# Kernel tuning notes

Hardware: AMD Instinct MI355X
Metric: run time of the kernel (lower is better)

Reference implementation:

```python
import jax, jax.numpy as jnp
import numpy as np

B, S, D = 1, 2048, 4096
H = 32
Q_RANK, KV_RANK = 1536, 512
NOPE, ROPE, VD = 128, 64, 128
QD = NOPE + ROPE  # 192
EPS = 1e-6
THETA = 10000.0


def setup_inputs() -> dict:
    key = jax.random.key(0)
    ks = jax.random.split(key, 8)
    std = 0.02
    return {
        'hidden_states': jax.random.normal(ks[0], (B, S, D), jnp.float32),
        'Wq_a': jax.random.normal(ks[1], (D, Q_RANK), jnp.float32) * std,
        'q_a_ln_w': jnp.ones((Q_RANK,), jnp.float32),
        'Wq_b': jax.random.normal(ks[2], (Q_RANK, H * QD), jnp.float32) * std,
        'Wkv_a': jax.random.normal(ks[3], (D, KV_RANK + ROPE), jnp.float32) * std,
        'kv_a_ln_w': jnp.ones((KV_RANK,), jnp.float32),
        'Wkv_b': jax.random.normal(ks[4], (KV_RANK, H * (NOPE + VD)), jnp.float32) * std,
        'Wo': jax.random.normal(ks[5], (H * VD, D), jnp.float32) * std,
    }


def _rmsnorm(x, w):
    return x * jax.lax.rsqrt(jnp.mean(x * x, axis=-1, keepdims=True) + EPS) * w


def _rotate_half(x):
    h = x.shape[-1] // 2
    return jnp.concatenate([-x[..., h:], x[..., :h]], axis=-1)


def _apply_rope(x, cos, sin):
    # DeepSeek interleave permutation: view(..., d//2, 2).transpose -> [evens | odds]
    xp = jnp.concatenate([x[..., 0::2], x[..., 1::2]], axis=-1)
    return xp * cos + _rotate_half(xp) * sin


def _mla_forward(hidden_states, Wq_a, q_a_ln_w, Wq_b, Wkv_a, kv_a_ln_w, Wkv_b, Wo):
    b, s, _ = hidden_states.shape
    # low-rank query projection
    q = _rmsnorm(hidden_states @ Wq_a, q_a_ln_w) @ Wq_b          # [b,s,H*QD]
    q = q.reshape(b, s, H, QD).transpose(0, 2, 1, 3)             # [b,H,s,QD]
    q_nope, q_pe = q[..., :NOPE], q[..., NOPE:]
    # compressed kv + shared rope key
    ckv = hidden_states @ Wkv_a                                   # [b,s,KV_RANK+ROPE]
    compressed, k_pe = ckv[..., :KV_RANK], ckv[..., KV_RANK:]
    kv = _rmsnorm(compressed, kv_a_ln_w) @ Wkv_b                 # [b,s,H*(NOPE+VD)]
    kv = kv.reshape(b, s, H, NOPE + VD).transpose(0, 2, 1, 3)    # [b,H,s,NOPE+VD]
    k_nope, v = kv[..., :NOPE], kv[..., NOPE:]
    k_pe = k_pe[:, None, :, :]                                    # [b,1,s,ROPE]
    # rotary tables (cos/sin duplicated halves)
    inv_freq = 1.0 / (THETA ** (jnp.arange(0, ROPE, 2, dtype=jnp.float32) / ROPE))
    freqs = jnp.outer(jnp.arange(s, dtype=jnp.float32), inv_freq)  # [s,ROPE/2]
    emb = jnp.concatenate([freqs, freqs], axis=-1)                 # [s,ROPE]
    cos = jnp.cos(emb)[None, None].astype(hidden_states.dtype)
    sin = jnp.sin(emb)[None, None].astype(hidden_states.dtype)
    q_pe = _apply_rope(q_pe, cos, sin)
    k_pe = _apply_rope(k_pe, cos, sin)
    # assemble full q/k heads
    qf = jnp.concatenate([q_nope, q_pe], axis=-1)                 # [b,H,s,QD]
    kf = jnp.concatenate([k_nope, jnp.broadcast_to(k_pe, (b, H, s, ROPE))], axis=-1)
    scale = QD ** (-0.5)
    scores = jnp.einsum('bhqd,bhkd->bhqk', qf, kf) * scale        # [b,H,s,s]
    causal = jnp.tril(jnp.ones((s, s), dtype=bool))
    scores = jnp.where(causal, scores, jnp.finfo(scores.dtype).min)
    probs = jax.nn.softmax(scores, axis=-1)
    o = jnp.einsum('bhqk,bhkd->bhqd', probs, v)                   # [b,H,s,VD]
    o = o.transpose(0, 2, 1, 3).reshape(b, s, H * VD)
    return o @ Wo


def reference(hidden_states, Wq_a, q_a_ln_w, Wq_b, Wkv_a, kv_a_ln_w, Wkv_b, Wo):
    return _mla_forward(hidden_states, Wq_a, q_a_ln_w, Wq_b, Wkv_a, kv_a_ln_w, Wkv_b, Wo)
```

## Files before the change

kernel.cpp:

```cpp
#include <hip/hip_runtime.h>

typedef unsigned short u16;
using bf16x8 = __attribute__((ext_vector_type(8))) __bf16;
using f32x4  = __attribute__((ext_vector_type(4))) float;
using s16x8  = __attribute__((ext_vector_type(8))) short;
using s16x4  = __attribute__((ext_vector_type(4))) short;

#define AS1 __attribute__((address_space(1)))
#define AS3 __attribute__((address_space(3)))

__device__ __forceinline__ void gload16(const u16* g, u16* l) {
  __builtin_amdgcn_global_load_lds((AS1 void*)(size_t)g, (AS3 void*)l, 16, 0, 0);
}

__device__ __forceinline__ u16 f2bf(float f) {
  unsigned u = __float_as_uint(f);
  u += 0x7fffu + ((u >> 16) & 1u);
  return (u16)(u >> 16);
}
__device__ __forceinline__ float bf2f(u16 h) {
  return __uint_as_float(((unsigned)h) << 16);
}

__device__ __forceinline__ void transpose_tile(const float* __restrict__ W,
                                               u16* __restrict__ WT,
                                               int K, int N, int nb, int kb,
                                               u16 (*tile)[72]) {
  const int t = threadIdx.x;
  const int rr = t >> 3;
  const int cc = (t & 7) * 8;
#pragma unroll
  for (int pass = 0; pass < 2; ++pass) {
    const float* src = W + (size_t)(kb + pass * 32 + rr) * N + nb + cc;
    float4 a = *reinterpret_cast<const float4*>(src);
    float4 b = *reinterpret_cast<const float4*>(src + 4);
    u16* tr = &tile[pass * 32 + rr][cc];
    tr[0] = f2bf(a.x); tr[1] = f2bf(a.y); tr[2] = f2bf(a.z); tr[3] = f2bf(a.w);
    tr[4] = f2bf(b.x); tr[5] = f2bf(b.y); tr[6] = f2bf(b.z); tr[7] = f2bf(b.w);
  }
  __syncthreads();
#pragma unroll
  for (int pass = 0; pass < 2; ++pass) {
    s16x8 v;
#pragma unroll
    for (int j = 0; j < 8; ++j) v[j] = (short)tile[cc + j][pass * 32 + rr];
    *reinterpret_cast<s16x8*>(WT + (size_t)(nb + pass * 32 + rr) * K + kb + cc) = v;
  }
}

__global__ __launch_bounds__(256) void prep_merged_kernel(
    const float* __restrict__ hs, u16* __restrict__ hs_bf,
    const float* __restrict__ Wqa, const float* __restrict__ Wkva, u16* __restrict__ WabT,
    const float* __restrict__ Wqb, u16* __restrict__ WqbT,
    const float* __restrict__ Wkvb, u16* __restrict__ WkvbT,
    const float* __restrict__ Wo, u16* __restrict__ WoT,
    float* __restrict__ cost, float* __restrict__ sint) {
  __shared__ u16 tile[64][72];
  const int bid = blockIdx.x, t = threadIdx.x;
  if (bid < 8192) {
    int i = (bid * 256 + t) * 4;
    float4 v = *reinterpret_cast<const float4*>(hs + i);
    s16x4 o;
    o[0] = (short)f2bf(v.x); o[1] = (short)f2bf(v.y);
    o[2] = (short)f2bf(v.z); o[3] = (short)f2bf(v.w);
    *reinterpret_cast<s16x4*>(hs_bf + i) = o;
  } else if (bid < 9728) {
    int r = bid - 8192;
    transpose_tile(Wqa, WabT, 4096, 1536, (r % 24) * 64, (r / 24) * 64, tile);
  } else if (bid < 10304) {
    int r = bid - 9728;
    transpose_tile(Wkva, WabT + (size_t)1536 * 4096, 4096, 576, (r % 9) * 64, (r / 9) * 64, tile);
  } else if (bid < 12608) {
    int r = bid - 10304;
    transpose_tile(Wqb, WqbT, 1536, 6144, (r % 96) * 64, (r / 96) * 64, tile);
  } else if (bid < 13632) {
    int r = bid - 12608;
    transpose_tile(Wkvb, WkvbT, 512, 8192, (r % 128) * 64, (r / 128) * 64, tile);
  } else if (bid < 17728) {
    int r = bid - 13632;
    transpose_tile(Wo, WoT, 4096, 4096, (r % 64) * 64, (r / 64) * 64, tile);
  } else {
    int idx = (bid - 17728) * 256 + t;
    int pos = idx >> 5, j = idx & 31;
    float inv = __expf(-(float)j * (9.210340371976184f / 32.0f));
    float f = (float)pos * inv;
    cost[idx] = cosf(f);
    sint[idx] = sinf(f);
  }
}

__global__ __launch_bounds__(256) void norms_merged_kernel(const u16* __restrict__ fused,
                                                           const float* __restrict__ qln,
                                                           const float* __restrict__ kvln,
                                                           u16* __restrict__ qan,
                                                           u16* __restrict__ cn) {
  const int bid = blockIdx.x, t = threadIdx.x;
  const int row = bid & 2047;
  const bool is_q = bid < 2048;
  const int R = is_q ? 1536 : 512;
  const u16* xr = fused + (size_t)row * 2112 + (is_q ? 0 : 1536);
  const float* w = is_q ? qln : kvln;
  u16* yr = (is_q ? qan + (size_t)row * 1536 : cn + (size_t)row * 512);
  float ss = 0.f;
  for (int i = t; i < R; i += 256) { float f = bf2f(xr[i]); ss += f * f; }
#pragma unroll
  for (int m = 32; m >= 1; m >>= 1) ss += __shfl_xor(ss, m);
  __shared__ float red[4];
  if ((t & 63) == 0) red[t >> 6] = ss;
  __syncthreads();
  float tot = red[0] + red[1] + red[2] + red[3];
  float r = rsqrtf(tot / (float)R + 1e-6f);
  for (int i = t; i < R; i += 256) yr[i] = f2bf(bf2f(xr[i]) * r * w[i]);
}

__global__ __launch_bounds__(256) void builds_merged_kernel(const u16* __restrict__ q,
                                                            const u16* __restrict__ ckv,
                                                            const float* __restrict__ cost,
                                                            const float* __restrict__ sint,
                                                            u16* __restrict__ qf,
                                                            u16* __restrict__ kf) {
  const int bid = blockIdx.x, t = threadIdx.x;
  if (bid < 6144) {
    int o8 = (bid * 256 + t) * 8;
    const float scale = 0.07216878364870323f;
    int c = (o8 % 192) >> 3;
    int rest = o8 / 192;
    int s = rest & 2047, h = rest >> 11;
    const u16* qrow = q + ((size_t)s * 32 + h) * 192;
    s16x8 out;
    if (c < 16) {
      s16x8 v = *reinterpret_cast<const s16x8*>(qrow + c * 8);
#pragma unroll
      for (int j = 0; j < 8; ++j) out[j] = (short)f2bf(bf2f((u16)v[j]) * scale);
    } else {
      int j0 = c * 8 - 128;
      bool lo = j0 < 32;
      int jj0 = lo ? j0 : j0 - 32;
      s16x8 a = *reinterpret_cast<const s16x8*>(qrow + 128 + 2 * jj0);
      s16x8 b = *reinterpret_cast<const s16x8*>(qrow + 128 + 2 * jj0 + 8);
      float4 c0 = *reinterpret_cast<const float4*>(cost + s * 32 + jj0);
      float4 c1 = *reinterpret_cast<const float4*>(cost + s * 32 + jj0 + 4);
      float4 s0 = *reinterpret_cast<const float4*>(sint + s * 32 + jj0);
      float4 s1 = *reinterpret_cast<const float4*>(sint + s * 32 + jj0 + 4);
      float cs[8] = {c0.x, c0.y, c0.z, c0.w, c1.x, c1.y, c1.z, c1.w};
      float sn[8] = {s0.x, s0.y, s0.z, s0.w, s1.x, s1.y, s1.z, s1.w};
#pragma unroll
      for (int j = 0; j < 8; ++j) {
        float x0 = bf2f((u16)((j < 4) ? a[2 * j] : b[2 * j - 8]));
        float x1 = bf2f((u16)((j < 4) ? a[2 * j + 1] : b[2 * j - 7]));
        float v = lo ? (x0 * cs[j] - x1 * sn[j]) : (x1 * cs[j] + x0 * sn[j]);
        out[j] = (short)f2bf(v * scale);
      }
    }
    *reinterpret_cast<s16x8*>(qf + o8) = out;
  } else {
    int o8 = ((bid - 6144) * 256 + t) * 8;
    int j0 = o8 & 63;
    int rest = o8 >> 6;
    int s = rest & 2047, h = rest >> 11;
    bool lo = j0 < 32;
    int jj0 = lo ? j0 : j0 - 32;
    const u16* crow = ckv + (size_t)s * 2112 + 512;
    s16x8 a = *reinterpret_cast<const s16x8*>(crow + 2 * jj0);
    s16x8 b = *reinterpret_cast<const s16x8*>(crow + 2 * jj0 + 8);
    float4 c0 = *reinterpret_cast<const float4*>(cost + s * 32 + jj0);
    float4 c1 = *reinterpret_cast<const float4*>(cost + s * 32 + jj0 + 4);
    float4 s0 = *reinterpret_cast<const float4*>(sint + s * 32 + jj0);
    float4 s1 = *reinterpret_cast<const float4*>(sint + s * 32 + jj0 + 4);
    float cs[8] = {c0.x, c0.y, c0.z, c0.w, c1.x, c1.y, c1.z, c1.w};
    float sn[8] = {s0.x, s0.y, s0.z, s0.w, s1.x, s1.y, s1.z, s1.w};
    s16x8 out;
#pragma unroll
    for (int j = 0; j < 8; ++j) {
      float x0 = bf2f((u16)((j < 4) ? a[2 * j] : b[2 * j - 8]));
      float x1 = bf2f((u16)((j < 4) ? a[2 * j + 1] : b[2 * j - 7]));
      float v = lo ? (x0 * cs[j] - x1 * sn[j]) : (x1 * cs[j] + x0 * sn[j]);
      out[j] = (short)f2bf(v);
    }
    *reinterpret_cast<s16x8*>(kf + ((size_t)h * 2048 + s) * 192 + 128 + j0) = out;
  }
}

template <int EPI>
__device__ __forceinline__ void gemm_v3_body(const u16* __restrict__ A,
                                             const u16* __restrict__ BT,
                                             void* __restrict__ Cv,
                                             void* __restrict__ Cv2,
                                             int M, int N, int K,
                                             int bx, int by, u16* S) {
  const int t0 = threadIdx.x;
  const int lane = t0 & 63, wave = t0 >> 6;
  const int wr = wave >> 1, wc = wave & 1;
  const int row0 = by * 128, col0 = bx * 128;
  const int lrow = lane & 15, lkg = lane >> 4;

  const int lp = lane ^ ((lane >> 3) & 3);
  const int srow_off = lp >> 2;
  const int skel = (lp & 3) * 8;
  const int c0 = wave * 2, c1 = c0 + 1;
  const int arow_c0 = row0 + c0 * 16 + srow_off;
  const int arow_c1 = row0 + c1 * 16 + srow_off;
  int brow_c0 = col0 + c0 * 16 + srow_off; if (brow_c0 > N - 1) brow_c0 = N - 1;
  int brow_c1 = col0 + c1 * 16 + srow_off; if (brow_c1 > N - 1) brow_c1 = N - 1;

  int aoff[4], boff[4];
#pragma unroll
  for (int m = 0; m < 4; ++m) {
    int r = wr * 64 + m * 16 + lrow;
    int off = r * 32 + lkg * 8;
    aoff[m] = off ^ ((off >> 3) & 0x18);
    r = wc * 64 + m * 16 + lrow;
    off = r * 32 + lkg * 8;
    boff[m] = off ^ ((off >> 3) & 0x18);
  }

  const int NT = K >> 5;

#pragma unroll
  for (int pt = 0; pt < 3; ++pt) {
    u16* ab = &S[pt * 8192];
    const int kb = pt * 32 + skel;
    gload16(A  + (size_t)arow_c0 * K + kb, ab + c0 * 512);
    gload16(A  + (size_t)arow_c1 * K + kb, ab + c1 * 512);
    gload16(BT + (size_t)brow_c0 * K + kb, ab + 4096 + c0 * 512);
    gload16(BT + (size_t)brow_c1 * K + kb, ab + 4096 + c1 * 512);
  }

  f32x4 acc[4][4];
#pragma unroll
  for (int m = 0; m < 4; ++m)
#pragma unroll
    for (int n = 0; n < 4; ++n) acc[m][n] = 0.f;

  for (int t = 0; t < NT; ++t) {
    if (t + 2 < NT)      asm volatile("s_waitcnt vmcnt(8)" ::: "memory");
    else if (t + 1 < NT) asm volatile("s_waitcnt vmcnt(4)" ::: "memory");
    else                 asm volatile("s_waitcnt vmcnt(0)" ::: "memory");
    __builtin_amdgcn_s_barrier();
    __builtin_amdgcn_sched_barrier(0);

    const u16* ab = &S[(t & 3) * 8192];
    bf16x8 af[4], bb[4];
#pragma unroll
    for (int m = 0; m < 4; ++m)
      af[m] = *reinterpret_cast<const bf16x8*>(ab + aoff[m]);
#pragma unroll
    for (int n = 0; n < 4; ++n)
      bb[n] = *reinterpret_cast<const bf16x8*>(ab + 4096 + boff[n]);

    if (t + 3 < NT) {
      u16* sb = &S[((t + 3) & 3) * 8192];
      const int kb = (t + 3) * 32 + skel;
      gload16(A  + (size_t)arow_c0 * K + kb, sb + c0 * 512);
      gload16(A  + (size_t)arow_c1 * K + kb, sb + c1 * 512);
      gload16(BT + (size_t)brow_c0 * K + kb, sb + 4096 + c0 * 512);
      gload16(BT + (size_t)brow_c1 * K + kb, sb + 4096 + c1 * 512);
    }

    __builtin_amdgcn_s_setprio(1);
#pragma unroll
    for (int m = 0; m < 4; ++m)
#pragma unroll
      for (int n = 0; n < 4; ++n)
        acc[m][n] = __builtin_amdgcn_mfma_f32_16x16x32_bf16(af[m], bb[n], acc[m][n], 0, 0, 0);
    __builtin_amdgcn_s_setprio(0);
  }

#pragma unroll
  for (int m = 0; m < 4; ++m) {
#pragma unroll
    for (int n = 0; n < 4; ++n) {
      int col = col0 + wc * 64 + n * 16 + lrow;
      int row = row0 + wr * 64 + m * 16 + lkg * 4;
      if (EPI == 2) {
        int d = col & 255, hh = col >> 8;
        if (d < 128) {
          u16* dst = (u16*)Cv + ((size_t)hh * 2048 + row) * 192 + d;
#pragma unroll
          for (int i = 0; i < 4; ++i) dst[(size_t)i * 192] = f2bf(acc[m][n][i]);
        } else {
          s16x4 v;
#pragma unroll
          for (int i = 0; i < 4; ++i) v[i] = (short)f2bf(acc[m][n][i]);
          *reinterpret_cast<s16x4*>((u16*)Cv2 + ((size_t)hh * 128 + (d - 128)) * 2048 + row) = v;
        }
      } else if (col < N) {
#pragma unroll
        for (int i = 0; i < 4; ++i) {
          size_t idx = (size_t)(row + i) * N + col;
          if (EPI == 1) ((u16*)Cv)[idx] = f2bf(acc[m][n][i]);
          else          ((float*)Cv)[idx] = acc[m][n][i];
        }
      }
    }
  }
}

template <int EPI>
__global__ __launch_bounds__(256) void gemm_v3_kernel(const u16* __restrict__ A,
                                                      const u16* __restrict__ BT,
                                                      void* __restrict__ Cv,
                                                      void* __restrict__ Cv2,
                                                      int M, int N, int K) {
  __shared__ __align__(16) u16 S[4 * 8192];
  gemm_v3_body<EPI>(A, BT, Cv, Cv2, M, N, K, blockIdx.x, blockIdx.y, S);
}

__global__ __launch_bounds__(256) void gemm_qkv_kernel(const u16* __restrict__ qan,
                                                       const u16* __restrict__ WqbT,
                                                       u16* __restrict__ qout,
                                                       const u16* __restrict__ cn,
                                                       const u16* __restrict__ WkvbT,
                                                       u16* __restrict__ kfb,
                                                       u16* __restrict__ vTb) {
  __shared__ __align__(16) u16 S[4 * 8192];
  if (blockIdx.z == 0) {
    if (blockIdx.x >= 48) return;
    gemm_v3_body<1>(qan, WqbT, qout, nullptr, 2048, 6144, 1536, blockIdx.x, blockIdx.y, S);
  } else {
    gemm_v3_body<2>(cn, WkvbT, kfb, vTb, 2048, 8192, 512, blockIdx.x, blockIdx.y, S);
  }
}

__global__ __launch_bounds__(256) void mla_attn_kernel(const u16* __restrict__ qf,
                                                       const u16* __restrict__ kf,
                                                       const u16* __restrict__ vT,
                                                       u16* __restrict__ o) {
  const int h = blockIdx.x, pair = blockIdx.y;
  const int t = threadIdx.x, wave = t >> 6, lane = t & 63;
  const int lrow = lane & 15, lkg = lane >> 4;
  __shared__ __align__(16) u16 Kt[2][12 * 512];
  __shared__ __align__(16) u16 Vt[2][8 * 512];
  __shared__ __align__(16) u16 Pl[4][16][36];

  const u16* ksrc[3]; u16 *kdst0[3], *kdst1[3];
#pragma unroll
  for (int i = 0; i < 3; ++i) {
    int c = wave * 3 + i, cg = c / 6, kk = c - cg * 6;
    ksrc[i] = kf + ((size_t)h * 2048 + cg * 16 + lrow) * 192 + kk * 32 + lkg * 8;
    kdst0[i] = &Kt[0][c * 512];
    kdst1[i] = &Kt[1][c * 512];
  }
  const u16* vsrc[2]; u16 *vdst0[2], *vdst1[2];
#pragma unroll
  for (int j = 0; j < 2; ++j) {
    int f = wave * 2 + j;
    vsrc[j] = vT + ((size_t)h * 128 + f * 16 + lrow) * 2048 + lkg * 8;
    vdst0[j] = &Vt[0][f * 512];
    vdst1[j] = &Vt[1][f * 512];
  }

  for (int qq = 0; qq < 2; ++qq) {
    const int qb = qq ? (31 - pair) : pair;
    const int qbase = qb * 64 + wave * 16;

    bf16x8 qfr[6];
    const u16* qrow_ptr = qf + ((size_t)h * 2048 + qbase + lrow) * 192;
#pragma unroll
    for (int kk = 0; kk < 6; ++kk)
      qfr[kk] = *reinterpret_cast<const bf16x8*>(qrow_ptr + kk * 32 + lkg * 8);

    f32x4 acc_o[8];
#pragma unroll
    for (int f = 0; f < 8; ++f) acc_o[f] = 0.f;
    float m_run[4], l_par[4];
#pragma unroll
    for (int i = 0; i < 4; ++i) { m_run[i] = -1e30f; l_par[i] = 0.f; }

    const int nt = 2 * qb + 2;

#pragma unroll
    for (int i = 0; i < 3; ++i) gload16(ksrc[i], kdst0[i]);
#pragma unroll
    for (int j = 0; j < 2; ++j) gload16(vsrc[j], vdst0[j]);

    for (int it = 0; it < nt; ++it) {
      const int kt = it * 32;
      if (it + 1 < nt) {
        const int nb = (it + 1) & 1;
        const size_t kadv = (size_t)(it + 1) * 32 * 192;
        const size_t vadv = (size_t)(it + 1) * 32;
#pragma unroll
        for (int i = 0; i < 3; ++i) gload16(ksrc[i] + kadv, nb ? kdst1[i] : kdst0[i]);
#pragma unroll
        for (int j = 0; j < 2; ++j) gload16(vsrc[j] + vadv, nb ? vdst1[j] : vdst0[j]);
        asm volatile("s_waitcnt vmcnt(5)" ::: "memory");
      } else {
        asm volatile("s_waitcnt vmcnt(0)" ::: "memory");
      }
      __builtin_amdgcn_s_barrier();
      __builtin_amdgcn_sched_barrier(0);

      const u16* Kb = &Kt[it & 1][0];
      const u16* Vb = &Vt[it & 1][0];
      if (kt <= qbase + 15) {
        f32x4 sv[2];
        sv[0] = 0.f; sv[1] = 0.f;
#pragma unroll
        for (int cg = 0; cg < 2; ++cg)
#pragma unroll
          for (int kk = 0; kk < 6; ++kk) {
            bf16x8 kfr = *reinterpret_cast<const bf16x8*>(&Kb[(cg * 6 + kk) * 512 + lane * 8]);
            sv[cg] = __builtin_amdgcn_mfma_f32_16x16x32_bf16(qfr[kk], kfr, sv[cg], 0, 0, 0);
          }
        const int qrow_b = qbase + lkg * 4;
        if (kt + 31 > qbase) {
#pragma unroll
          for (int cg = 0; cg < 2; ++cg) {
            int kvcol = kt + cg * 16 + lrow;
#pragma unroll
            for (int i = 0; i < 4; ++i)
              if (kvcol > qrow_b + i) sv[cg][i] = -__builtin_inff();
          }
        }
        float tmax[4];
#pragma unroll
        for (int i = 0; i < 4; ++i) tmax[i] = fmaxf(sv[0][i], sv[1][i]);
#pragma unroll
        for (int m = 8; m >= 1; m >>= 1)
#pragma unroll
          for (int i = 0; i < 4; ++i) tmax[i] = fmaxf(tmax[i], __shfl_xor(tmax[i], m));
        int need = 0;
#pragma unroll
        for (int i = 0; i < 4; ++i) need |= (tmax[i] > m_run[i] + 8.f) ? 1 : 0;
        if (__any(need)) {
#pragma unroll
          for (int i = 0; i < 4; ++i) {
            float mnew = fmaxf(m_run[i], tmax[i]);
            float alpha = __expf(m_run[i] - mnew);
            m_run[i] = mnew;
            l_par[i] *= alpha;
#pragma unroll
            for (int f = 0; f < 8; ++f) acc_o[f][i] *= alpha;
          }
        }
#pragma unroll
        for (int i = 0; i < 4; ++i) {
          sv[0][i] = __expf(sv[0][i] - m_run[i]);
          sv[1][i] = __expf(sv[1][i] - m_run[i]);
          l_par[i] += sv[0][i] + sv[1][i];
        }
#pragma unroll
        for (int cg = 0; cg < 2; ++cg)
#pragma unroll
          for (int i = 0; i < 4; ++i)
            Pl[wave][lkg * 4 + i][cg * 16 + lrow] = f2bf(sv[cg][i]);
        bf16x8 pf = *reinterpret_cast<const bf16x8*>(&Pl[wave][lrow][lkg * 8]);
#pragma unroll
        for (int f = 0; f < 8; ++f) {
          bf16x8 vfr = *reinterpret_cast<const bf16x8*>(&Vb[f * 512 + lane * 8]);
          acc_o[f] = __builtin_amdgcn_mfma_f32_16x16x32_bf16(pf, vfr, acc_o[f], 0, 0, 0);
        }
      }
      __builtin_amdgcn_sched_barrier(0);
      __builtin_amdgcn_s_barrier();
    }
#pragma unroll
    for (int i = 0; i < 4; ++i)
#pragma unroll
      for (int m = 8; m >= 1; m >>= 1) l_par[i] += __shfl_xor(l_par[i], m);
#pragma unroll
    for (int f = 0; f < 8; ++f)
#pragma unroll
      for (int i = 0; i < 4; ++i) {
        int row = qbase + lkg * 4 + i;
        int col = h * 128 + f * 16 + lrow;
        o[(size_t)row * 4096 + col] = f2bf(acc_o[f][i] / l_par[i]);
      }
  }
}

extern "C" void kernel_launch(void* const* d_in, const int* in_sizes, int n_in,
                              void* d_out, int out_size, void* d_ws, size_t ws_size,
                              hipStream_t stream) {
  (void)in_sizes; (void)n_in; (void)out_size; (void)ws_size;
  const float* hs   = (const float*)d_in[0];
  const float* Wqa  = (const float*)d_in[1];
  const float* qln  = (const float*)d_in[2];
  const float* Wqb  = (const float*)d_in[3];
  const float* Wkva = (const float*)d_in[4];
  const float* kvln = (const float*)d_in[5];
  const float* Wkvb = (const float*)d_in[6];
  const float* Wo   = (const float*)d_in[7];
  float* out = (float*)d_out;

  char* p = (char*)d_ws;
  size_t off = 0;
  auto carve = [&](size_t bytes) {
    char* r = p + off;
    off += (bytes + 255) & ~(size_t)255;
    return r;
  };
  u16* hs_bf = (u16*)carve((size_t)2048 * 4096 * 2);
  u16* WabT  = (u16*)carve((size_t)2112 * 4096 * 2);
  u16* WqbT  = (u16*)carve((size_t)6144 * 1536 * 2);
  u16* WkvbT = (u16*)carve((size_t)8192 * 512 * 2);
  u16* WoT   = (u16*)carve((size_t)4096 * 4096 * 2);
  u16* fused = (u16*)carve((size_t)2048 * 2112 * 2);
  u16* qan   = (u16*)carve((size_t)2048 * 1536 * 2);
  u16* q     = (u16*)carve((size_t)2048 * 6144 * 2);
  u16* cn    = (u16*)carve((size_t)2048 * 512 * 2);
  u16* qfb   = (u16*)carve((size_t)32 * 2048 * 192 * 2);
  u16* kfb   = (u16*)carve((size_t)32 * 2048 * 192 * 2);
  u16* vTb   = (u16*)carve((size_t)32 * 128 * 2048 * 2);
  u16* ob    = (u16*)carve((size_t)2048 * 4096 * 2);
  float* cost = (float*)carve((size_t)65536 * 4);
  float* sint = (float*)carve((size_t)65536 * 4);

  prep_merged_kernel<<<17984, 256, 0, stream>>>(hs, hs_bf, Wqa, Wkva, WabT,
                                                Wqb, WqbT, Wkvb, WkvbT, Wo, WoT,
                                                cost, sint);

  gemm_v3_kernel<1><<<dim3(17, 16), 256, 0, stream>>>(hs_bf, WabT, fused, nullptr, 2048, 2112, 4096);

  norms_merged_kernel<<<4096, 256, 0, stream>>>(fused, qln, kvln, qan, cn);

  gemm_qkv_kernel<<<dim3(64, 16, 2), 256, 0, stream>>>(qan, WqbT, q, cn, WkvbT, kfb, vTb);

  builds_merged_kernel<<<8192, 256, 0, stream>>>(q, fused + 1536, cost, sint, qfb, kfb);

  mla_attn_kernel<<<dim3(32, 16), 256, 0, stream>>>(qfb, kfb, vTb, ob);

  gemm_v3_kernel<0><<<dim3(32, 16), 256, 0, stream>>>(ob, WoT, out, nullptr, 2048, 4096, 4096);
}
```

Measured before the change: 403.1 us.

## Add 128x256-tile triple-buffered GEMM for QKV up-projection and output projection

Introduces a new GEMM body with 128x256 output tiles, each wave computing 64x128, and a three-stage LDS ring buffer with explicit vmcnt waits. It replaces the previous 128x128 GEMM for the Q/KV up-projection and the final Wo projection, with grids halved to match. The larger tile raises arithmetic intensity and B-fragment reuse per A load, and the deeper pipeline hides global-load latency. In exchange it doubles accumulator registers per thread, which risks lower occupancy or spills, and the launch bounds now request two blocks per CU. Fewer blocks on 256 CUs also worsens wave-quantization, e.g. the Wo GEMM drops to 256 blocks.

```diff
diff --git a/kernel.cpp b/kernel.cpp
--- a/kernel.cpp
+++ b/kernel.cpp
@@ -272,19 +272,7 @@
     for (int n = 0; n < 4; ++n) {
       int col = col0 + wc * 64 + n * 16 + lrow;
       int row = row0 + wr * 64 + m * 16 + lkg * 4;
-      if (EPI == 2) {
-        int d = col & 255, hh = col >> 8;
-        if (d < 128) {
-          u16* dst = (u16*)Cv + ((size_t)hh * 2048 + row) * 192 + d;
-#pragma unroll
-          for (int i = 0; i < 4; ++i) dst[(size_t)i * 192] = f2bf(acc[m][n][i]);
-        } else {
-          s16x4 v;
-#pragma unroll
-          for (int i = 0; i < 4; ++i) v[i] = (short)f2bf(acc[m][n][i]);
-          *reinterpret_cast<s16x4*>((u16*)Cv2 + ((size_t)hh * 128 + (d - 128)) * 2048 + row) = v;
-        }
-      } else if (col < N) {
+      if (col < N) {
 #pragma unroll
         for (int i = 0; i < 4; ++i) {
           size_t idx = (size_t)(row + i) * N + col;
@@ -306,19 +294,157 @@
   gemm_v3_body<EPI>(A, BT, Cv, Cv2, M, N, K, blockIdx.x, blockIdx.y, S);
 }
 
-__global__ __launch_bounds__(256) void gemm_qkv_kernel(const u16* __restrict__ qan,
-                                                       const u16* __restrict__ WqbT,
-                                                       u16* __restrict__ qout,
-                                                       const u16* __restrict__ cn,
-                                                       const u16* __restrict__ WkvbT,
-                                                       u16* __restrict__ kfb,
-                                                       u16* __restrict__ vTb) {
-  __shared__ __align__(16) u16 S[4 * 8192];
+template <int EPI>
+__device__ __forceinline__ void gemm_v4_body(const u16* __restrict__ A,
+                                             const u16* __restrict__ BT,
+                                             void* __restrict__ Cv,
+                                             void* __restrict__ Cv2,
+                                             int M, int N, int K,
+                                             int bx, int by, u16* S) {
+  const int t0 = threadIdx.x;
+  const int lane = t0 & 63, wave = t0 >> 6;
+  const int wr = wave >> 1, wc = wave & 1;
+  const int row0 = by * 128, col0 = bx * 256;
+  const int lrow = lane & 15, lkg = lane >> 4;
+
+  const int lp = lane ^ ((lane >> 3) & 3);
+  const int srow_off = lp >> 2;
+  const int skel = (lp & 3) * 8;
+
+  const int ac0 = wave * 2, ac1 = ac0 + 1;
+  const int arow_0 = row0 + ac0 * 16 + srow_off;
+  const int arow_1 = row0 + ac1 * 16 + srow_off;
+  int brow[4];
+#pragma unroll
+  for (int j = 0; j < 4; ++j) {
+    int r = col0 + (wave * 4 + j) * 16 + srow_off;
+    brow[j] = (r > N - 1) ? (N - 1) : r;
+  }
+
+  int aoff[4], boff[8];
+#pragma unroll
+  for (int m = 0; m < 4; ++m) {
+    int r = wr * 64 + m * 16 + lrow;
+    int off = r * 32 + lkg * 8;
+    aoff[m] = off ^ ((off >> 3) & 0x18);
+  }
+#pragma unroll
+  for (int n = 0; n < 8; ++n) {
+    int r = wc * 128 + n * 16 + lrow;
+    int off = r * 32 + lkg * 8;
+    boff[n] = off ^ ((off >> 3) & 0x18);
+  }
+
+  const int NT = K >> 5;
+
+#pragma unroll
+  for (int pt = 0; pt < 2; ++pt) {
+    u16* sb = &S[pt * 12288];
+    const int kb = pt * 32 + skel;
+    gload16(A + (size_t)arow_0 * K + kb, sb + ac0 * 512);
+    gload16(A + (size_t)arow_1 * K + kb, sb + ac1 * 512);
+#pragma unroll
+    for (int j = 0; j < 4; ++j)
+      gload16(BT + (size_t)brow[j] * K + kb, sb + 4096 + (wave * 4 + j) * 512);
+  }
+
+  f32x4 acc[4][8];
+#pragma unroll
+  for (int m = 0; m < 4; ++m)
+#pragma unroll
+    for (int n = 0; n < 8; ++n) acc[m][n] = 0.f;
+
+  int bufr = 0, bufw = 2;
+  for (int t = 0; t < NT; ++t) {
+    if (t + 2 < NT) {
+      u16* sb = &S[bufw * 12288];
+      const int kb = (t + 2) * 32 + skel;
+      gload16(A + (size_t)arow_0 * K + kb, sb + ac0 * 512);
+      gload16(A + (size_t)arow_1 * K + kb, sb + ac1 * 512);
+#pragma unroll
+      for (int j = 0; j < 4; ++j)
+        gload16(BT + (size_t)brow[j] * K + kb, sb + 4096 + (wave * 4 + j) * 512);
+      bufw = (bufw + 1 == 3) ? 0 : bufw + 1;
+      asm volatile("s_waitcnt vmcnt(12)" ::: "memory");
+    } else if (t + 1 < NT) {
+      asm volatile("s_waitcnt vmcnt(6)" ::: "memory");
+    } else {
+      asm volatile("s_waitcnt vmcnt(0)" ::: "memory");
+    }
+    __builtin_amdgcn_s_barrier();
+    __builtin_amdgcn_sched_barrier(0);
+
+    const u16* ab = &S[bufr * 12288];
+    bufr = (bufr + 1 == 3) ? 0 : bufr + 1;
+    bf16x8 af[4];
+#pragma unroll
+    for (int m = 0; m < 4; ++m)
+      af[m] = *reinterpret_cast<const bf16x8*>(ab + aoff[m]);
+
+    __builtin_amdgcn_s_setprio(1);
+#pragma unroll
+    for (int n = 0; n < 8; ++n) {
+      bf16x8 bbn = *reinterpret_cast<const bf16x8*>(ab + 4096 + boff[n]);
+#pragma unroll
+      for (int m = 0; m < 4; ++m)
+        acc[m][n] = __builtin_amdgcn_mfma_f32_16x16x32_bf16(af[m], bbn, acc[m][n], 0, 0, 0);
+    }
+    __builtin_amdgcn_s_setprio(0);
+  }
+
+#pragma unroll
+  for (int m = 0; m < 4; ++m) {
+#pragma unroll
+    for (int n = 0; n < 8; ++n) {
+      int col = col0 + wc * 128 + n * 16 + lrow;
+      int row = row0 + wr * 64 + m * 16 + lkg * 4;
+      if (EPI == 2) {
+        int d = col & 255, hh = col >> 8;
+        if (d < 128) {
+          u16* dst = (u16*)Cv + ((size_t)hh * 2048 + row) * 192 + d;
+#pragma unroll
+          for (int i = 0; i < 4; ++i) dst[(size_t)i * 192] = f2bf(acc[m][n][i]);
+        } else {
+          s16x4 v;
+#pragma unroll
+          for (int i = 0; i < 4; ++i) v[i] = (short)f2bf(acc[m][n][i]);
+          *reinterpret_cast<s16x4*>((u16*)Cv2 + ((size_t)hh * 128 + (d - 128)) * 2048 + row) = v;
+        }
+      } else if (col < N) {
+#pragma unroll
+        for (int i = 0; i < 4; ++i) {
+          size_t idx = (size_t)(row + i) * N + col;
+          if (EPI == 1) ((u16*)Cv)[idx] = f2bf(acc[m][n][i]);
+          else          ((float*)Cv)[idx] = acc[m][n][i];
+        }
+      }
+    }
+  }
+}
+
+template <int EPI>
+__global__ __launch_bounds__(256, 2) void gemm_v4_kernel(const u16* __restrict__ A,
+                                                         const u16* __restrict__ BT,
+                                                         void* __restrict__ Cv,
+                                                         void* __restrict__ Cv2,
+                                                         int M, int N, int K) {
+  __shared__ __align__(16) u16 S[3 * 12288];
+  gemm_v4_body<EPI>(A, BT, Cv, Cv2, M, N, K, blockIdx.x, blockIdx.y, S);
+}
+
+__global__ __launch_bounds__(256, 2) void gemm_qkv_kernel(const u16* __restrict__ qan,
+                                                          const u16* __restrict__ WqbT,
+                                                          u16* __restrict__ qout,
+                                                          const u16* __restrict__ cn,
+                                                          const u16* __restrict__ WkvbT,
+                                                          u16* __restrict__ kfb,
+                                                          u16* __restrict__ vTb) {
+  __shared__ __align__(16) u16 S[3 * 12288];
   if (blockIdx.z == 0) {
-    if (blockIdx.x >= 48) return;
-    gemm_v3_body<1>(qan, WqbT, qout, nullptr, 2048, 6144, 1536, blockIdx.x, blockIdx.y, S);
+    if (blockIdx.x >= 24) return;
+    gemm_v4_body<1>(qan, WqbT, qout, nullptr, 2048, 6144, 1536, blockIdx.x, blockIdx.y, S);
   } else {
-    gemm_v3_body<2>(cn, WkvbT, kfb, vTb, 2048, 8192, 512, blockIdx.x, blockIdx.y, S);
+    gemm_v4_body<2>(cn, WkvbT, kfb, vTb, 2048, 8192, 512, blockIdx.x, blockIdx.y, S);
   }
 }
 
@@ -515,11 +641,11 @@
 
   norms_merged_kernel<<<4096, 256, 0, stream>>>(fused, qln, kvln, qan, cn);
 
-  gemm_qkv_kernel<<<dim3(64, 16, 2), 256, 0, stream>>>(qan, WqbT, q, cn, WkvbT, kfb, vTb);
+  gemm_qkv_kernel<<<dim3(32, 16, 2), 256, 0, stream>>>(qan, WqbT, q, cn, WkvbT, kfb, vTb);
 
   builds_merged_kernel<<<8192, 256, 0, stream>>>(q, fused + 1536, cost, sint, qfb, kfb);
 
   mla_attn_kernel<<<dim3(32, 16), 256, 0, stream>>>(qfb, kfb, vTb, ob);
 
-  gemm_v3_kernel<0><<<dim3(32, 16), 256, 0, stream>>>(ob, WoT, out, nullptr, 2048, 4096, 4096);
-}
+  gemm_v4_kernel<0><<<dim3(16, 16), 256, 0, stream>>>(ob, WoT, out, nullptr, 2048, 4096, 4096);
+}
```

Measured after the change: 399.1 us. No clear change (-1.0%).
